# Kernel tuning notes

Measured on AMD Instinct MI355X. Metric: run time of the kernel, lower is better.

## Reference

```python
import jax, jax.numpy as jnp
import numpy as np

B, S, D, H = 1, 4096, 1024, 16
DH = D // H

def setup_inputs() -> dict:
    key = jax.random.key(0)
    ks = jax.random.split(key, 5)
    std = float(np.sqrt(2.0 / (D + D)))
    return {
        "x": jax.random.normal(ks[0], (B, S, D), dtype=jnp.float32),
        "Wq": jax.random.normal(ks[1], (D, D), dtype=jnp.float32) * std,
        "Wk": jax.random.normal(ks[2], (D, D), dtype=jnp.float32) * std,
        "Wv": jax.random.normal(ks[3], (D, D), dtype=jnp.float32) * std,
        "Wo": jax.random.normal(ks[4], (D, D), dtype=jnp.float32) * std,
    }

def reference(x, Wq, Wk, Wv, Wo):
    # projections: input @ W.T, then split heads: b s (h d) -> b h s d
    def split_heads(t):
        b, s, _ = t.shape
        return t.reshape(b, s, H, DH).transpose(0, 2, 1, 3)
    q = split_heads(x @ Wq.T)
    k = split_heads(x @ Wk.T)
    v = split_heads(x @ Wv.T)
    scale = 1.0 / jnp.sqrt(jnp.asarray(DH, dtype=x.dtype))
    scores = jnp.einsum("bhqd,bhkd->bhqk", q, k) * scale  # (b,h,s,s)
    # causal mask: allow k <= q
    causal = jnp.tril(jnp.ones((S, S), dtype=bool))
    scores = jnp.where(causal, scores, jnp.finfo(scores.dtype).min)
    attn = jax.nn.softmax(scores, axis=-1)
    out = jnp.einsum("bhqk,bhkd->bhqd", attn, v)  # (b,h,s,d)
    out = out.transpose(0, 2, 1, 3).reshape(B, S, D)  # b h s d -> b s (h d)
    return out @ Wo.T
```

## Files before the change

### kernel.cpp

```cpp
#include <hip/hip_runtime.h>
#include <math.h>

#define SEQ 4096
#define DM  1024
#define NH  16
#define DH  64

typedef _Float16 h16;
typedef __attribute__((ext_vector_type(4))) _Float16 h16x4;
typedef __attribute__((ext_vector_type(8))) _Float16 h16x8;
typedef __attribute__((ext_vector_type(4))) float f32x4;

__global__ __launch_bounds__(256) void cvt_f32_f16(const float* __restrict__ in,
                                                   h16* __restrict__ out, int n4) {
    const int i = blockIdx.x * 256 + threadIdx.x;
    if (i < n4) {
        const float4 v = ((const float4*)in)[i];
        h16x4 o = { (h16)v.x, (h16)v.y, (h16)v.z, (h16)v.w };
        ((h16x4*)out)[i] = o;
    }
}

#define GST 40

__global__ __launch_bounds__(256, 2) void gemm_qkv(const h16* __restrict__ xh,
                                                   const h16* __restrict__ Wq,
                                                   const h16* __restrict__ Wk,
                                                   const h16* __restrict__ Wv,
                                                   h16* __restrict__ Qh,
                                                   h16* __restrict__ Kh,
                                                   h16* __restrict__ Vth,
                                                   float scl) {
    __shared__ h16 As[2][64 * GST];
    __shared__ h16 Bs[2][128 * GST];

    const int z    = blockIdx.z;
    const h16* B   = (z == 0) ? Wq : (z == 1) ? Wk : Wv;
    const int t    = threadIdx.x;
    const int lane = t & 63;
    const int w    = t >> 6;
    const int wm   = (w >> 1) * 32;
    const int wn   = (w & 1) * 64;
    const int l15  = lane & 15;
    const int lq   = lane >> 4;
    const int lq8  = lq * 8;
    const int m0   = blockIdx.y * 64;
    const int n0   = blockIdx.x * 128;
    const int K    = DM, M = SEQ, N = DM;

    const int arow = t >> 2;
    const int ac8  = (t & 3) * 8;

    f32x4 acc[2][4] = {};

    const h16* pA  = xh + (size_t)(m0 + arow) * K + ac8;
    const h16* pB0 = B + (size_t)(n0 + arow) * K + ac8;
    const h16* pB1 = B + (size_t)(n0 + 64 + arow) * K + ac8;

    h16x8 ra = *(const h16x8*)pA;
    h16x8 rb0 = *(const h16x8*)pB0;
    h16x8 rb1 = *(const h16x8*)pB1;

    for (int k0 = 0; k0 < K; k0 += 32) {
        const int p = (k0 >> 5) & 1;
        *(h16x8*)&As[p][arow * GST + ac8]        = ra;
        *(h16x8*)&Bs[p][arow * GST + ac8]        = rb0;
        *(h16x8*)&Bs[p][(64 + arow) * GST + ac8] = rb1;
        __syncthreads();
        if (k0 + 32 < K) {
            ra  = *(const h16x8*)(pA + k0 + 32);
            rb0 = *(const h16x8*)(pB0 + k0 + 32);
            rb1 = *(const h16x8*)(pB1 + k0 + 32);
        }
        h16x8 af[2], bf[4];
        #pragma unroll
        for (int i = 0; i < 2; ++i)
            af[i] = *(const h16x8*)&As[p][(wm + i * 16 + l15) * GST + lq8];
        #pragma unroll
        for (int j = 0; j < 4; ++j)
            bf[j] = *(const h16x8*)&Bs[p][(wn + j * 16 + l15) * GST + lq8];
        #pragma unroll
        for (int i = 0; i < 2; ++i)
            #pragma unroll
            for (int j = 0; j < 4; ++j)
                acc[i][j] = __builtin_amdgcn_mfma_f32_16x16x32_f16(af[i], bf[j], acc[i][j], 0, 0, 0);
    }

    const int cr = wm + lq * 4;
    const int cc = wn + l15;
    if (z == 2) {
        #pragma unroll
        for (int i = 0; i < 2; ++i)
            #pragma unroll
            for (int j = 0; j < 4; ++j) {
                const int gm0 = m0 + cr + i * 16;
                const int gn  = n0 + cc + j * 16;
                h16x4 v = { (h16)acc[i][j][0], (h16)acc[i][j][1],
                            (h16)acc[i][j][2], (h16)acc[i][j][3] };
                *(h16x4*)(Vth + (size_t)gn * M + gm0) = v;
            }
    } else {
        h16* Og = (z == 0) ? Qh : Kh;
        const float e = (z == 0) ? scl : 1.0f;
        #pragma unroll
        for (int i = 0; i < 2; ++i)
            #pragma unroll
            for (int j = 0; j < 4; ++j)
                #pragma unroll
                for (int r = 0; r < 4; ++r) {
                    const int gm = m0 + cr + i * 16 + r;
                    const int gn = n0 + cc + j * 16;
                    Og[(size_t)gm * N + gn] = (h16)(acc[i][j][r] * e);
                }
    }
}

__global__ __launch_bounds__(256, 2) void gemm_out(const h16* __restrict__ A,
                                                   const h16* __restrict__ B,
                                                   float* __restrict__ C) {
    __shared__ h16 As[2][64 * GST];
    __shared__ h16 Bs[2][128 * GST];

    const int t    = threadIdx.x;
    const int lane = t & 63;
    const int w    = t >> 6;
    const int wm   = (w >> 1) * 32;
    const int wn   = (w & 1) * 64;
    const int l15  = lane & 15;
    const int lq   = lane >> 4;
    const int lq8  = lq * 8;
    const int m0   = blockIdx.y * 64;
    const int n0   = blockIdx.x * 128;
    const int K    = DM, N = DM;

    const int arow = t >> 2;
    const int ac8  = (t & 3) * 8;

    f32x4 acc[2][4] = {};

    const h16* pA  = A + (size_t)(m0 + arow) * K + ac8;
    const h16* pB0 = B + (size_t)(n0 + arow) * K + ac8;
    const h16* pB1 = B + (size_t)(n0 + 64 + arow) * K + ac8;

    h16x8 ra = *(const h16x8*)pA;
    h16x8 rb0 = *(const h16x8*)pB0;
    h16x8 rb1 = *(const h16x8*)pB1;

    for (int k0 = 0; k0 < K; k0 += 32) {
        const int p = (k0 >> 5) & 1;
        *(h16x8*)&As[p][arow * GST + ac8]        = ra;
        *(h16x8*)&Bs[p][arow * GST + ac8]        = rb0;
        *(h16x8*)&Bs[p][(64 + arow) * GST + ac8] = rb1;
        __syncthreads();
        if (k0 + 32 < K) {
            ra  = *(const h16x8*)(pA + k0 + 32);
            rb0 = *(const h16x8*)(pB0 + k0 + 32);
            rb1 = *(const h16x8*)(pB1 + k0 + 32);
        }
        h16x8 af[2], bf[4];
        #pragma unroll
        for (int i = 0; i < 2; ++i)
            af[i] = *(const h16x8*)&As[p][(wm + i * 16 + l15) * GST + lq8];
        #pragma unroll
        for (int j = 0; j < 4; ++j)
            bf[j] = *(const h16x8*)&Bs[p][(wn + j * 16 + l15) * GST + lq8];
        #pragma unroll
        for (int i = 0; i < 2; ++i)
            #pragma unroll
            for (int j = 0; j < 4; ++j)
                acc[i][j] = __builtin_amdgcn_mfma_f32_16x16x32_f16(af[i], bf[j], acc[i][j], 0, 0, 0);
    }

    const int cr = wm + lq * 4;
    const int cc = wn + l15;
    #pragma unroll
    for (int i = 0; i < 2; ++i)
        #pragma unroll
        for (int j = 0; j < 4; ++j)
            #pragma unroll
            for (int r = 0; r < 4; ++r)
                C[(size_t)(m0 + cr + i * 16 + r) * N + n0 + cc + j * 16] = acc[i][j][r];
}

#define AST 72

__device__ __forceinline__ void tile_softmax(f32x4 s[4], float& m_st, float& l_st,
                                             f32x4 o[4], h16* ps_row, bool diag,
                                             int q_loc, int lq) {
    if (diag) {
        #pragma unroll
        for (int jj = 0; jj < 4; ++jj)
            #pragma unroll
            for (int r = 0; r < 4; ++r)
                if ((jj * 16 + lq * 4 + r) > q_loc) s[jj][r] = -1e30f;
    }
    float mx = m_st;
    #pragma unroll
    for (int jj = 0; jj < 4; ++jj)
        #pragma unroll
        for (int r = 0; r < 4; ++r)
            mx = fmaxf(mx, s[jj][r]);
    mx = fmaxf(mx, __shfl_xor(mx, 16, 64));
    mx = fmaxf(mx, __shfl_xor(mx, 32, 64));
    const float alpha = exp2f(m_st - mx);
    m_st = mx;
    float sum = 0.0f;
    #pragma unroll
    for (int jj = 0; jj < 4; ++jj) {
        const float p0 = exp2f(s[jj][0] - mx);
        const float p1 = exp2f(s[jj][1] - mx);
        const float p2 = exp2f(s[jj][2] - mx);
        const float p3 = exp2f(s[jj][3] - mx);
        sum += (p0 + p1) + (p2 + p3);
        h16x4 pk = { (h16)p0, (h16)p1, (h16)p2, (h16)p3 };
        *(h16x4*)(ps_row + jj * 16 + lq * 4) = pk;
    }
    sum += __shfl_xor(sum, 16, 64);
    sum += __shfl_xor(sum, 32, 64);
    l_st = l_st * alpha + sum;
    #pragma unroll
    for (int jj = 0; jj < 4; ++jj)
        #pragma unroll
        for (int r = 0; r < 4; ++r)
            o[jj][r] *= alpha;
}

__global__ __launch_bounds__(256, 2) void flash_attn_mfma(
        const h16* __restrict__ Qg, const h16* __restrict__ Kg,
        const h16* __restrict__ Vt, h16* __restrict__ Og) {
    __shared__ h16 Ks[2][64 * AST];
    __shared__ h16 Vs[2][64 * AST];
    __shared__ h16 Ps[2][64 * AST];

    const int qA   = blockIdx.x;
    const int qB   = 63 - qA;
    const int hh   = blockIdx.y;
    const int t    = threadIdx.x;
    const int lane = t & 63;
    const int w    = t >> 6;
    const int l15  = lane & 15;
    const int lq   = lane >> 4;
    const int lq8  = lq * 8;
    const int hc   = hh * DH;
    const int q_loc = w * 16 + l15;

    const int r1 = t >> 3;
    const int r2 = r1 + 32;
    const int c1 = (t & 7) * 8;

    {
        const int qa0 = qA * 64, qb0 = qB * 64;
        *(h16x8*)&Ks[0][r1 * AST + c1] = *(const h16x8*)(Qg + (size_t)(qa0 + r1) * DM + hc + c1);
        *(h16x8*)&Ks[0][r2 * AST + c1] = *(const h16x8*)(Qg + (size_t)(qa0 + r2) * DM + hc + c1);
        *(h16x8*)&Vs[0][r1 * AST + c1] = *(const h16x8*)(Qg + (size_t)(qb0 + r1) * DM + hc + c1);
        *(h16x8*)&Vs[0][r2 * AST + c1] = *(const h16x8*)(Qg + (size_t)(qb0 + r2) * DM + hc + c1);
    }
    h16x8 kv1 = *(const h16x8*)(Kg + (size_t)(r1) * DM + hc + c1);
    h16x8 kv2 = *(const h16x8*)(Kg + (size_t)(r2) * DM + hc + c1);
    h16x8 vv1 = *(const h16x8*)(Vt + (size_t)(hc + r1) * SEQ + c1);
    h16x8 vv2 = *(const h16x8*)(Vt + (size_t)(hc + r2) * SEQ + c1);

    __syncthreads();
    h16x8 qfA[2], qfB[2];
    qfA[0] = *(const h16x8*)&Ks[0][q_loc * AST + lq8];
    qfA[1] = *(const h16x8*)&Ks[0][q_loc * AST + 32 + lq8];
    qfB[0] = *(const h16x8*)&Vs[0][q_loc * AST + lq8];
    qfB[1] = *(const h16x8*)&Vs[0][q_loc * AST + 32 + lq8];
    __syncthreads();

    float mA = -1e30f, lA = 0.0f, mB = -1e30f, lB = 0.0f;
    f32x4 oA[4] = {}, oB[4] = {};
    h16* const psA = &Ps[0][(size_t)q_loc * AST];
    h16* const psB = &Ps[1][(size_t)q_loc * AST];

    for (int kt = 0; kt <= qB; ++kt) {
        h16* const Ksb = &Ks[kt & 1][0];
        h16* const Vsb = &Vs[kt & 1][0];
        *(h16x8*)&Ksb[r1 * AST + c1] = kv1;
        *(h16x8*)&Ksb[r2 * AST + c1] = kv2;
        *(h16x8*)&Vsb[r1 * AST + c1] = vv1;
        *(h16x8*)&Vsb[r2 * AST + c1] = vv2;
        __syncthreads();
        if (kt < qB) {
            const int k0n = (kt + 1) * 64;
            kv1 = *(const h16x8*)(Kg + (size_t)(k0n + r1) * DM + hc + c1);
            kv2 = *(const h16x8*)(Kg + (size_t)(k0n + r2) * DM + hc + c1);
            vv1 = *(const h16x8*)(Vt + (size_t)(hc + r1) * SEQ + k0n + c1);
            vv2 = *(const h16x8*)(Vt + (size_t)(hc + r2) * SEQ + k0n + c1);
        }
        const bool doA = (kt <= qA);

        f32x4 sA[4] = {}, sB[4] = {};
        #pragma unroll
        for (int kc = 0; kc < 2; ++kc)
            #pragma unroll
            for (int jj = 0; jj < 4; ++jj) {
                const h16x8 kf = *(const h16x8*)&Ksb[(jj * 16 + l15) * AST + kc * 32 + lq8];
                if (doA) sA[jj] = __builtin_amdgcn_mfma_f32_16x16x32_f16(kf, qfA[kc], sA[jj], 0, 0, 0);
                sB[jj] = __builtin_amdgcn_mfma_f32_16x16x32_f16(kf, qfB[kc], sB[jj], 0, 0, 0);
            }

        if (doA) tile_softmax(sA, mA, lA, oA, psA, kt == qA, q_loc, lq);
        tile_softmax(sB, mB, lB, oB, psB, kt == qB, q_loc, lq);

        asm volatile("s_waitcnt lgkmcnt(0)" ::: "memory");
        h16x8 pfA[2], pfB[2];
        if (doA) {
            pfA[0] = *(const h16x8*)(psA + lq8);
            pfA[1] = *(const h16x8*)(psA + 32 + lq8);
        }
        pfB[0] = *(const h16x8*)(psB + lq8);
        pfB[1] = *(const h16x8*)(psB + 32 + lq8);

        #pragma unroll
        for (int kc = 0; kc < 2; ++kc)
            #pragma unroll
            for (int jj = 0; jj < 4; ++jj) {
                const h16x8 vf = *(const h16x8*)&Vsb[(jj * 16 + l15) * AST + kc * 32 + lq8];
                if (doA) oA[jj] = __builtin_amdgcn_mfma_f32_16x16x32_f16(vf, pfA[kc], oA[jj], 0, 0, 0);
                oB[jj] = __builtin_amdgcn_mfma_f32_16x16x32_f16(vf, pfB[kc], oB[jj], 0, 0, 0);
            }
    }

    {
        const float il = 1.0f / lA;
        const size_t qg = (size_t)(qA * 64 + q_loc) * DM + hc;
        #pragma unroll
        for (int jj = 0; jj < 4; ++jj) {
            h16x4 ov = { (h16)(oA[jj][0] * il), (h16)(oA[jj][1] * il),
                         (h16)(oA[jj][2] * il), (h16)(oA[jj][3] * il) };
            *(h16x4*)(Og + qg + jj * 16 + lq * 4) = ov;
        }
    }
    {
        const float il = 1.0f / lB;
        const size_t qg = (size_t)(qB * 64 + q_loc) * DM + hc;
        #pragma unroll
        for (int jj = 0; jj < 4; ++jj) {
            h16x4 ov = { (h16)(oB[jj][0] * il), (h16)(oB[jj][1] * il),
                         (h16)(oB[jj][2] * il), (h16)(oB[jj][3] * il) };
            *(h16x4*)(Og + qg + jj * 16 + lq * 4) = ov;
        }
    }
}

extern "C" void kernel_launch(void* const* d_in, const int* in_sizes, int n_in,
                              void* d_out, int out_size, void* d_ws, size_t ws_size,
                              hipStream_t stream) {
    const float* x  = (const float*)d_in[0];
    const float* Wq = (const float*)d_in[1];
    const float* Wk = (const float*)d_in[2];
    const float* Wv = (const float*)d_in[3];
    const float* Wo = (const float*)d_in[4];
    float* out = (float*)d_out;

    const size_t SD = (size_t)SEQ * DM;
    const size_t DD = (size_t)DM * DM;

    h16* xh  = (h16*)d_ws;
    h16* wqh = xh + SD;
    h16* wkh = wqh + DD;
    h16* wvh = wkh + DD;
    h16* woh = wvh + DD;
    h16* Qh  = woh + DD;
    h16* Kh  = Qh + SD;
    h16* Vth = Kh + SD;
    h16* AOh = Vth + SD;

    cvt_f32_f16<<<(int)(SD / 4 / 256), 256, 0, stream>>>(x,  xh,  (int)(SD / 4));
    cvt_f32_f16<<<(int)(DD / 4 / 256), 256, 0, stream>>>(Wq, wqh, (int)(DD / 4));
    cvt_f32_f16<<<(int)(DD / 4 / 256), 256, 0, stream>>>(Wk, wkh, (int)(DD / 4));
    cvt_f32_f16<<<(int)(DD / 4 / 256), 256, 0, stream>>>(Wv, wvh, (int)(DD / 4));
    cvt_f32_f16<<<(int)(DD / 4 / 256), 256, 0, stream>>>(Wo, woh, (int)(DD / 4));

    const dim3 blk(256);

    const float SCL = 0.125f * 1.44269504088896340736f;

    gemm_qkv<<<dim3(DM / 128, SEQ / 64, 3), blk, 0, stream>>>(
        xh, wqh, wkh, wvh, Qh, Kh, Vth, SCL);

    flash_attn_mfma<<<dim3(32, NH), blk, 0, stream>>>(Qh, Kh, Vth, AOh);

    gemm_out<<<dim3(DM / 128, SEQ / 64), blk, 0, stream>>>(AOh, woh, out);
}
```

Baseline: 263.5 us.

## Use direct global-to-LDS loads with larger GEMM tiles; split attention loop by causal range

Both GEMMs now stage tiles with global_load_lds straight into unpadded LDS and grow the block tile from 64x128 to 128x128, so each wave computes a 64x64 sub-tile. Register prefetching and LDS double buffering go away, which makes every K step wait for its loads. The attention kernel drops K/V double buffering to single buffers with an extra barrier and moves the LDS stride from 72 to 80. It raises occupancy to 3 blocks per SM and splits the key loop into a paired-tile phase and a B-only phase, removing the per-iteration doA branches.

New measurement: 237.2 us. 10.0% less time.

```diff
diff --git a/kernel.cpp b/kernel.cpp
--- a/kernel.cpp
+++ b/kernel.cpp
@@ -10,6 +10,12 @@
 typedef __attribute__((ext_vector_type(4))) _Float16 h16x4;
 typedef __attribute__((ext_vector_type(8))) _Float16 h16x8;
 typedef __attribute__((ext_vector_type(4))) float f32x4;
+
+__device__ __forceinline__ void gload_lds16(const h16* g, h16* l) {
+    __builtin_amdgcn_global_load_lds(
+        (const __attribute__((address_space(1))) void*)g,
+        (__attribute__((address_space(3))) void*)l, 16, 0, 0);
+}
 
 __global__ __launch_bounds__(256) void cvt_f32_f16(const float* __restrict__ in,
                                                    h16* __restrict__ out, int n4) {
@@ -21,66 +27,63 @@
     }
 }
 
-#define GST 40
-
-__global__ __launch_bounds__(256, 2) void gemm_qkv(const h16* __restrict__ xh,
-                                                   const h16* __restrict__ Wq,
-                                                   const h16* __restrict__ Wk,
-                                                   const h16* __restrict__ Wv,
-                                                   h16* __restrict__ Qh,
-                                                   h16* __restrict__ Kh,
-                                                   h16* __restrict__ Vth,
-                                                   float scl) {
-    __shared__ h16 As[2][64 * GST];
-    __shared__ h16 Bs[2][128 * GST];
+#define GT 32
+
+__global__ __launch_bounds__(256) void gemm_qkv(const h16* __restrict__ xh,
+                                                const h16* __restrict__ Wq,
+                                                const h16* __restrict__ Wk,
+                                                const h16* __restrict__ Wv,
+                                                h16* __restrict__ Qh,
+                                                h16* __restrict__ Kh,
+                                                h16* __restrict__ Vth,
+                                                float scl) {
+    __shared__ h16 As[128 * GT];
+    __shared__ h16 Bs[128 * GT];
 
     const int z    = blockIdx.z;
     const h16* B   = (z == 0) ? Wq : (z == 1) ? Wk : Wv;
     const int t    = threadIdx.x;
     const int lane = t & 63;
     const int w    = t >> 6;
-    const int wm   = (w >> 1) * 32;
+    const int wm   = (w >> 1) * 64;
     const int wn   = (w & 1) * 64;
     const int l15  = lane & 15;
     const int lq   = lane >> 4;
     const int lq8  = lq * 8;
-    const int m0   = blockIdx.y * 64;
+    const int m0   = blockIdx.y * 128;
     const int n0   = blockIdx.x * 128;
-    const int K    = DM, M = SEQ, N = DM;
-
-    const int arow = t >> 2;
-    const int ac8  = (t & 3) * 8;
-
-    f32x4 acc[2][4] = {};
-
-    const h16* pA  = xh + (size_t)(m0 + arow) * K + ac8;
-    const h16* pB0 = B + (size_t)(n0 + arow) * K + ac8;
-    const h16* pB1 = B + (size_t)(n0 + 64 + arow) * K + ac8;
-
-    h16x8 ra = *(const h16x8*)pA;
-    h16x8 rb0 = *(const h16x8*)pB0;
-    h16x8 rb1 = *(const h16x8*)pB1;
+    const int K = DM, M = SEQ, N = DM;
+
+    const int srow = w * 16 + (lane >> 2);
+    const int scol = (lane & 3) * 8;
+    const h16* pa0 = xh + (size_t)(m0 + srow) * K + scol;
+    const h16* pa1 = xh + (size_t)(m0 + 64 + srow) * K + scol;
+    const h16* pb0 = B  + (size_t)(n0 + srow) * K + scol;
+    const h16* pb1 = B  + (size_t)(n0 + 64 + srow) * K + scol;
+    h16* const la0 = &As[w * 512];
+    h16* const la1 = &As[2048 + w * 512];
+    h16* const lb0 = &Bs[w * 512];
+    h16* const lb1 = &Bs[2048 + w * 512];
+
+    f32x4 acc[4][4] = {};
 
     for (int k0 = 0; k0 < K; k0 += 32) {
-        const int p = (k0 >> 5) & 1;
-        *(h16x8*)&As[p][arow * GST + ac8]        = ra;
-        *(h16x8*)&Bs[p][arow * GST + ac8]        = rb0;
-        *(h16x8*)&Bs[p][(64 + arow) * GST + ac8] = rb1;
-        __syncthreads();
-        if (k0 + 32 < K) {
-            ra  = *(const h16x8*)(pA + k0 + 32);
-            rb0 = *(const h16x8*)(pB0 + k0 + 32);
-            rb1 = *(const h16x8*)(pB1 + k0 + 32);
-        }
-        h16x8 af[2], bf[4];
-        #pragma unroll
-        for (int i = 0; i < 2; ++i)
-            af[i] = *(const h16x8*)&As[p][(wm + i * 16 + l15) * GST + lq8];
+        __syncthreads();
+        gload_lds16(pa0 + k0, la0);
+        gload_lds16(pa1 + k0, la1);
+        gload_lds16(pb0 + k0, lb0);
+        gload_lds16(pb1 + k0, lb1);
+        __syncthreads();
+
+        h16x8 af[4], bf[4];
+        #pragma unroll
+        for (int i = 0; i < 4; ++i)
+            af[i] = *(const h16x8*)&As[(wm + i * 16 + l15) * GT + lq8];
         #pragma unroll
         for (int j = 0; j < 4; ++j)
-            bf[j] = *(const h16x8*)&Bs[p][(wn + j * 16 + l15) * GST + lq8];
-        #pragma unroll
-        for (int i = 0; i < 2; ++i)
+            bf[j] = *(const h16x8*)&Bs[(wn + j * 16 + l15) * GT + lq8];
+        #pragma unroll
+        for (int i = 0; i < 4; ++i)
             #pragma unroll
             for (int j = 0; j < 4; ++j)
                 acc[i][j] = __builtin_amdgcn_mfma_f32_16x16x32_f16(af[i], bf[j], acc[i][j], 0, 0, 0);
@@ -90,7 +93,7 @@
     const int cc = wn + l15;
     if (z == 2) {
         #pragma unroll
-        for (int i = 0; i < 2; ++i)
+        for (int i = 0; i < 4; ++i)
             #pragma unroll
             for (int j = 0; j < 4; ++j) {
                 const int gm0 = m0 + cr + i * 16;
@@ -103,7 +106,7 @@
         h16* Og = (z == 0) ? Qh : Kh;
         const float e = (z == 0) ? scl : 1.0f;
         #pragma unroll
-        for (int i = 0; i < 2; ++i)
+        for (int i = 0; i < 4; ++i)
             #pragma unroll
             for (int j = 0; j < 4; ++j)
                 #pragma unroll
@@ -115,57 +118,54 @@
     }
 }
 
-__global__ __launch_bounds__(256, 2) void gemm_out(const h16* __restrict__ A,
-                                                   const h16* __restrict__ B,
-                                                   float* __restrict__ C) {
-    __shared__ h16 As[2][64 * GST];
-    __shared__ h16 Bs[2][128 * GST];
+__global__ __launch_bounds__(256) void gemm_out(const h16* __restrict__ A,
+                                                const h16* __restrict__ B,
+                                                float* __restrict__ C) {
+    __shared__ h16 As[128 * GT];
+    __shared__ h16 Bs[128 * GT];
 
     const int t    = threadIdx.x;
     const int lane = t & 63;
     const int w    = t >> 6;
-    const int wm   = (w >> 1) * 32;
+    const int wm   = (w >> 1) * 64;
     const int wn   = (w & 1) * 64;
     const int l15  = lane & 15;
     const int lq   = lane >> 4;
     const int lq8  = lq * 8;
-    const int m0   = blockIdx.y * 64;
+    const int m0   = blockIdx.y * 128;
     const int n0   = blockIdx.x * 128;
-    const int K    = DM, N = DM;
-
-    const int arow = t >> 2;
-    const int ac8  = (t & 3) * 8;
-
-    f32x4 acc[2][4] = {};
-
-    const h16* pA  = A + (size_t)(m0 + arow) * K + ac8;
-    const h16* pB0 = B + (size_t)(n0 + arow) * K + ac8;
-    const h16* pB1 = B + (size_t)(n0 + 64 + arow) * K + ac8;
-
-    h16x8 ra = *(const h16x8*)pA;
-    h16x8 rb0 = *(const h16x8*)pB0;
-    h16x8 rb1 = *(const h16x8*)pB1;
+    const int K = DM, N = DM;
+
+    const int srow = w * 16 + (lane >> 2);
+    const int scol = (lane & 3) * 8;
+    const h16* pa0 = A + (size_t)(m0 + srow) * K + scol;
+    const h16* pa1 = A + (size_t)(m0 + 64 + srow) * K + scol;
+    const h16* pb0 = B + (size_t)(n0 + srow) * K + scol;
+    const h16* pb1 = B + (size_t)(n0 + 64 + srow) * K + scol;
+    h16* const la0 = &As[w * 512];
+    h16* const la1 = &As[2048 + w * 512];
+    h16* const lb0 = &Bs[w * 512];
+    h16* const lb1 = &Bs[2048 + w * 512];
+
+    f32x4 acc[4][4] = {};
 
     for (int k0 = 0; k0 < K; k0 += 32) {
-        const int p = (k0 >> 5) & 1;
-        *(h16x8*)&As[p][arow * GST + ac8]        = ra;
-        *(h16x8*)&Bs[p][arow * GST + ac8]        = rb0;
-        *(h16x8*)&Bs[p][(64 + arow) * GST + ac8] = rb1;
-        __syncthreads();
-        if (k0 + 32 < K) {
-            ra  = *(const h16x8*)(pA + k0 + 32);
-            rb0 = *(const h16x8*)(pB0 + k0 + 32);
-            rb1 = *(const h16x8*)(pB1 + k0 + 32);
-        }
-        h16x8 af[2], bf[4];
-        #pragma unroll
-        for (int i = 0; i < 2; ++i)
-            af[i] = *(const h16x8*)&As[p][(wm + i * 16 + l15) * GST + lq8];
+        __syncthreads();
+        gload_lds16(pa0 + k0, la0);
+        gload_lds16(pa1 + k0, la1);
+        gload_lds16(pb0 + k0, lb0);
+        gload_lds16(pb1 + k0, lb1);
+        __syncthreads();
+
+        h16x8 af[4], bf[4];
+        #pragma unroll
+        for (int i = 0; i < 4; ++i)
+            af[i] = *(const h16x8*)&As[(wm + i * 16 + l15) * GT + lq8];
         #pragma unroll
         for (int j = 0; j < 4; ++j)
-            bf[j] = *(const h16x8*)&Bs[p][(wn + j * 16 + l15) * GST + lq8];
-        #pragma unroll
-        for (int i = 0; i < 2; ++i)
+            bf[j] = *(const h16x8*)&Bs[(wn + j * 16 + l15) * GT + lq8];
+        #pragma unroll
+        for (int i = 0; i < 4; ++i)
             #pragma unroll
             for (int j = 0; j < 4; ++j)
                 acc[i][j] = __builtin_amdgcn_mfma_f32_16x16x32_f16(af[i], bf[j], acc[i][j], 0, 0, 0);
@@ -174,7 +174,7 @@
     const int cr = wm + lq * 4;
     const int cc = wn + l15;
     #pragma unroll
-    for (int i = 0; i < 2; ++i)
+    for (int i = 0; i < 4; ++i)
         #pragma unroll
         for (int j = 0; j < 4; ++j)
             #pragma unroll
@@ -182,7 +182,7 @@
                 C[(size_t)(m0 + cr + i * 16 + r) * N + n0 + cc + j * 16] = acc[i][j][r];
 }
 
-#define AST 72
+#define AST 80
 
 __device__ __forceinline__ void tile_softmax(f32x4 s[4], float& m_st, float& l_st,
                                              f32x4 o[4], h16* ps_row, bool diag,
@@ -225,11 +225,11 @@
             o[jj][r] *= alpha;
 }
 
-__global__ __launch_bounds__(256, 2) void flash_attn_mfma(
+__global__ __launch_bounds__(256, 3) void flash_attn_mfma(
         const h16* __restrict__ Qg, const h16* __restrict__ Kg,
         const h16* __restrict__ Vt, h16* __restrict__ Og) {
-    __shared__ h16 Ks[2][64 * AST];
-    __shared__ h16 Vs[2][64 * AST];
+    __shared__ h16 Ks[64 * AST];
+    __shared__ h16 Vs[64 * AST];
     __shared__ h16 Ps[2][64 * AST];
 
     const int qA   = blockIdx.x;
@@ -250,10 +250,10 @@
 
     {
         const int qa0 = qA * 64, qb0 = qB * 64;
-        *(h16x8*)&Ks[0][r1 * AST + c1] = *(const h16x8*)(Qg + (size_t)(qa0 + r1) * DM + hc + c1);
-        *(h16x8*)&Ks[0][r2 * AST + c1] = *(const h16x8*)(Qg + (size_t)(qa0 + r2) * DM + hc + c1);
-        *(h16x8*)&Vs[0][r1 * AST + c1] = *(const h16x8*)(Qg + (size_t)(qb0 + r1) * DM + hc + c1);
-        *(h16x8*)&Vs[0][r2 * AST + c1] = *(const h16x8*)(Qg + (size_t)(qb0 + r2) * DM + hc + c1);
+        *(h16x8*)&Ks[r1 * AST + c1] = *(const h16x8*)(Qg + (size_t)(qa0 + r1) * DM + hc + c1);
+        *(h16x8*)&Ks[r2 * AST + c1] = *(const h16x8*)(Qg + (size_t)(qa0 + r2) * DM + hc + c1);
+        *(h16x8*)&Vs[r1 * AST + c1] = *(const h16x8*)(Qg + (size_t)(qb0 + r1) * DM + hc + c1);
+        *(h16x8*)&Vs[r2 * AST + c1] = *(const h16x8*)(Qg + (size_t)(qb0 + r2) * DM + hc + c1);
     }
     h16x8 kv1 = *(const h16x8*)(Kg + (size_t)(r1) * DM + hc + c1);
     h16x8 kv2 = *(const h16x8*)(Kg + (size_t)(r2) * DM + hc + c1);
@@ -262,24 +262,67 @@
 
     __syncthreads();
     h16x8 qfA[2], qfB[2];
-    qfA[0] = *(const h16x8*)&Ks[0][q_loc * AST + lq8];
-    qfA[1] = *(const h16x8*)&Ks[0][q_loc * AST + 32 + lq8];
-    qfB[0] = *(const h16x8*)&Vs[0][q_loc * AST + lq8];
-    qfB[1] = *(const h16x8*)&Vs[0][q_loc * AST + 32 + lq8];
-    __syncthreads();
+    qfA[0] = *(const h16x8*)&Ks[q_loc * AST + lq8];
+    qfA[1] = *(const h16x8*)&Ks[q_loc * AST + 32 + lq8];
+    qfB[0] = *(const h16x8*)&Vs[q_loc * AST + lq8];
+    qfB[1] = *(const h16x8*)&Vs[q_loc * AST + 32 + lq8];
 
     float mA = -1e30f, lA = 0.0f, mB = -1e30f, lB = 0.0f;
     f32x4 oA[4] = {}, oB[4] = {};
     h16* const psA = &Ps[0][(size_t)q_loc * AST];
     h16* const psB = &Ps[1][(size_t)q_loc * AST];
 
-    for (int kt = 0; kt <= qB; ++kt) {
-        h16* const Ksb = &Ks[kt & 1][0];
-        h16* const Vsb = &Vs[kt & 1][0];
-        *(h16x8*)&Ksb[r1 * AST + c1] = kv1;
-        *(h16x8*)&Ksb[r2 * AST + c1] = kv2;
-        *(h16x8*)&Vsb[r1 * AST + c1] = vv1;
-        *(h16x8*)&Vsb[r2 * AST + c1] = vv2;
+    int kt = 0;
+    for (; kt <= qA; ++kt) {
+        __syncthreads();
+        *(h16x8*)&Ks[r1 * AST + c1] = kv1;
+        *(h16x8*)&Ks[r2 * AST + c1] = kv2;
+        *(h16x8*)&Vs[r1 * AST + c1] = vv1;
+        *(h16x8*)&Vs[r2 * AST + c1] = vv2;
+        __syncthreads();
+        {
+            const int k0n = (kt + 1) * 64;
+            kv1 = *(const h16x8*)(Kg + (size_t)(k0n + r1) * DM + hc + c1);
+            kv2 = *(const h16x8*)(Kg + (size_t)(k0n + r2) * DM + hc + c1);
+            vv1 = *(const h16x8*)(Vt + (size_t)(hc + r1) * SEQ + k0n + c1);
+            vv2 = *(const h16x8*)(Vt + (size_t)(hc + r2) * SEQ + k0n + c1);
+        }
+
+        f32x4 sA[4] = {}, sB[4] = {};
+        #pragma unroll
+        for (int kc = 0; kc < 2; ++kc)
+            #pragma unroll
+            for (int jj = 0; jj < 4; ++jj) {
+                const h16x8 kf = *(const h16x8*)&Ks[(jj * 16 + l15) * AST + kc * 32 + lq8];
+                sA[jj] = __builtin_amdgcn_mfma_f32_16x16x32_f16(kf, qfA[kc], sA[jj], 0, 0, 0);
+                sB[jj] = __builtin_amdgcn_mfma_f32_16x16x32_f16(kf, qfB[kc], sB[jj], 0, 0, 0);
+            }
+
+        tile_softmax(sA, mA, lA, oA, psA, kt == qA, q_loc, lq);
+        tile_softmax(sB, mB, lB, oB, psB, false, q_loc, lq);
+
+        asm volatile("s_waitcnt lgkmcnt(0)" ::: "memory");
+        h16x8 pfA[2], pfB[2];
+        pfA[0] = *(const h16x8*)(psA + lq8);
+        pfA[1] = *(const h16x8*)(psA + 32 + lq8);
+        pfB[0] = *(const h16x8*)(psB + lq8);
+        pfB[1] = *(const h16x8*)(psB + 32 + lq8);
+
+        #pragma unroll
+        for (int kc = 0; kc < 2; ++kc)
+            #pragma unroll
+            for (int jj = 0; jj < 4; ++jj) {
+                const h16x8 vf = *(const h16x8*)&Vs[(jj * 16 + l15) * AST + kc * 32 + lq8];
+                oA[jj] = __builtin_amdgcn_mfma_f32_16x16x32_f16(vf, pfA[kc], oA[jj], 0, 0, 0);
+                oB[jj] = __builtin_amdgcn_mfma_f32_16x16x32_f16(vf, pfB[kc], oB[jj], 0, 0, 0);
+            }
+    }
+    for (; kt <= qB; ++kt) {
+        __syncthreads();
+        *(h16x8*)&Ks[r1 * AST + c1] = kv1;
+        *(h16x8*)&Ks[r2 * AST + c1] = kv2;
+        *(h16x8*)&Vs[r1 * AST + c1] = vv1;
+        *(h16x8*)&Vs[r2 * AST + c1] = vv2;
         __syncthreads();
         if (kt < qB) {
             const int k0n = (kt + 1) * 64;
@@ -288,27 +331,20 @@
             vv1 = *(const h16x8*)(Vt + (size_t)(hc + r1) * SEQ + k0n + c1);
             vv2 = *(const h16x8*)(Vt + (size_t)(hc + r2) * SEQ + k0n + c1);
         }
-        const bool doA = (kt <= qA);
-
-        f32x4 sA[4] = {}, sB[4] = {};
+
+        f32x4 sB[4] = {};
         #pragma unroll
         for (int kc = 0; kc < 2; ++kc)
             #pragma unroll
             for (int jj = 0; jj < 4; ++jj) {
-                const h16x8 kf = *(const h16x8*)&Ksb[(jj * 16 + l15) * AST + kc * 32 + lq8];
-                if (doA) sA[jj] = __builtin_amdgcn_mfma_f32_16x16x32_f16(kf, qfA[kc], sA[jj], 0, 0, 0);
+                const h16x8 kf = *(const h16x8*)&Ks[(jj * 16 + l15) * AST + kc * 32 + lq8];
                 sB[jj] = __builtin_amdgcn_mfma_f32_16x16x32_f16(kf, qfB[kc], sB[jj], 0, 0, 0);
             }
 
-        if (doA) tile_softmax(sA, mA, lA, oA, psA, kt == qA, q_loc, lq);
         tile_softmax(sB, mB, lB, oB, psB, kt == qB, q_loc, lq);
 
         asm volatile("s_waitcnt lgkmcnt(0)" ::: "memory");
-        h16x8 pfA[2], pfB[2];
-        if (doA) {
-            pfA[0] = *(const h16x8*)(psA + lq8);
-            pfA[1] = *(const h16x8*)(psA + 32 + lq8);
-        }
+        h16x8 pfB[2];
         pfB[0] = *(const h16x8*)(psB + lq8);
         pfB[1] = *(const h16x8*)(psB + 32 + lq8);
 
@@ -316,8 +352,7 @@
         for (int kc = 0; kc < 2; ++kc)
             #pragma unroll
             for (int jj = 0; jj < 4; ++jj) {
-                const h16x8 vf = *(const h16x8*)&Vsb[(jj * 16 + l15) * AST + kc * 32 + lq8];
-                if (doA) oA[jj] = __builtin_amdgcn_mfma_f32_16x16x32_f16(vf, pfA[kc], oA[jj], 0, 0, 0);
+                const h16x8 vf = *(const h16x8*)&Vs[(jj * 16 + l15) * AST + kc * 32 + lq8];
                 oB[jj] = __builtin_amdgcn_mfma_f32_16x16x32_f16(vf, pfB[kc], oB[jj], 0, 0, 0);
             }
     }
@@ -377,10 +412,10 @@
 
     const float SCL = 0.125f * 1.44269504088896340736f;
 
-    gemm_qkv<<<dim3(DM / 128, SEQ / 64, 3), blk, 0, stream>>>(
+    gemm_qkv<<<dim3(DM / 128, SEQ / 128, 3), blk, 0, stream>>>(
         xh, wqh, wkh, wvh, Qh, Kh, Vth, SCL);
 
     flash_attn_mfma<<<dim3(32, NH), blk, 0, stream>>>(Qh, Kh, Vth, AOh);
 
-    gemm_out<<<dim3(DM / 128, SEQ / 64), blk, 0, stream>>>(AOh, woh, out);
-}
+    gemm_out<<<dim3(DM / 128, SEQ / 128), blk, 0, stream>>>(AOh, woh, out);
+}
```
